# Kernel tuning notes

Measured on AMD Instinct MI355X. Metric: run time of the kernel, lower is better.

## Reference

```python
import jax, jax.numpy as jnp
import numpy as np

D_MODEL = 512
HEADS = 8
D_FF = 1024
EPS = 1e-5


def layer_norm(x, gamma, beta):
    mu = jnp.mean(x, axis=-1, keepdims=True)
    var = jnp.mean(jnp.square(x - mu), axis=-1, keepdims=True)
    return (x - mu) * jax.lax.rsqrt(var + EPS) * gamma + beta


def mha(q, k, v, mask=None):
    # q,k,v: [B, S, D]; no input/output projections in the original module
    B, Sq, D = q.shape
    Sk = k.shape[1]
    dk = D // HEADS
    qh = q.reshape(B, Sq, HEADS, dk).transpose(0, 2, 1, 3)  # [B,H,Sq,dk]
    kh = k.reshape(B, Sk, HEADS, dk).transpose(0, 2, 1, 3)
    vh = v.reshape(B, Sk, HEADS, dk).transpose(0, 2, 1, 3)
    scores = jnp.einsum('bhqd,bhkd->bhqk', qh, kh) / np.sqrt(dk).astype(q.dtype)
    if mask is not None:
        scores = jnp.where(mask == 0, jnp.asarray(-1e9, scores.dtype), scores)
    attn = jax.nn.softmax(scores, axis=-1)  # dropout is identity in eval mode
    out = jnp.einsum('bhqk,bhkd->bhqd', attn, vh)
    return out.transpose(0, 2, 1, 3).reshape(B, Sq, D)


def setup_inputs() -> dict:
    key = jax.random.key(0)
    ks = jax.random.split(key, 8)
    B, S = 4, 2048
    x = jax.random.normal(ks[0], (B, S, D_MODEL), dtype=jnp.float32)
    encoder_output = jax.random.normal(ks[1], (B, S, D_MODEL), dtype=jnp.float32)
    mask = jax.random.randint(ks[2], (B, 1, S, S), 0, 2, dtype=jnp.int32)
    params = {
        'ln1_g': jnp.ones((D_MODEL,), jnp.float32), 'ln1_b': jnp.zeros((D_MODEL,), jnp.float32),
        'ln2_g': jnp.ones((D_MODEL,), jnp.float32), 'ln2_b': jnp.zeros((D_MODEL,), jnp.float32),
        'ln3_g': jnp.ones((D_MODEL,), jnp.float32), 'ln3_b': jnp.zeros((D_MODEL,), jnp.float32),
        'W1': jax.random.normal(ks[3], (D_MODEL, D_FF), jnp.float32) * (1.0 / np.sqrt(D_MODEL)),
        'b1': jnp.zeros((D_FF,), jnp.float32),
        'W2': jax.random.normal(ks[4], (D_FF, D_MODEL), jnp.float32) * (1.0 / np.sqrt(D_FF)),
        'b2': jnp.zeros((D_MODEL,), jnp.float32),
    }
    return {'x': x, 'encoder_output': encoder_output, 'mask': mask, **params}


def reference(x, encoder_output, mask, ln1_g, ln1_b, ln2_g, ln2_b, ln3_g, ln3_b, W1, b1, W2, b2):
    # pre-norm masked self-attention + residual (dropout = identity, eval mode)
    x1 = layer_norm(x, ln1_g, ln1_b)
    x = x + mha(x1, x1, x1, mask)
    # pre-norm cross-attention + residual
    x1 = layer_norm(x, ln2_g, ln2_b)
    x = x + mha(x1, encoder_output, encoder_output, None)
    # pre-norm FFN + residual
    x1 = layer_norm(x, ln3_g, ln3_b)
    h = jax.nn.relu(x1 @ W1 + b1)
    x = x + (h @ W2 + b2)
    return x
```

## Files before the change

### kernel.cpp

```cpp
#include <hip/hip_runtime.h>
#include <hip/hip_bf16.h>

#define D_MODEL 512
#define HEADS   8
#define DK      64
#define D_FF    1024
#define SEQ     2048
#define BATCH   4
#define NTOK    (BATCH*SEQ)
#define NELEM   (NTOK*D_MODEL)

#define QSCALE  0.18033688011112042f
#define MFIX    40.0f

typedef __attribute__((ext_vector_type(8))) short bf8_t;
typedef __attribute__((ext_vector_type(4))) float f4_t;

#define GLD16(gp, lp) __builtin_amdgcn_global_load_lds( \
    (const __attribute__((address_space(1))) void*)(gp), \
    (__attribute__((address_space(3))) void*)(lp), 16, 0, 0)

__device__ __forceinline__ float ldf(const void* p, size_t i, int f32) {
    return f32 ? ((const float*)p)[i] : __bfloat162float(((const __hip_bfloat16*)p)[i]);
}
__device__ __forceinline__ short f2bf(float f) {
    union { __hip_bfloat16 h; short s; } u; u.h = __float2bfloat16(f); return u.s;
}
__device__ __forceinline__ float bf2f(short s) {
    return __uint_as_float(((unsigned)(unsigned short)s) << 16);
}
__device__ __forceinline__ unsigned fbits(float f) { return __float_as_uint(f); }

__device__ __forceinline__ float fast_exp2(float x) {
    float r; asm("v_exp_f32 %0, %1" : "=v"(r) : "v"(x)); return r;
}

__global__ void detect_k(const uint4* __restrict__ w, int* __restrict__ flags) {
    __shared__ int found;
    if (threadIdx.x == 0) found = 0;
    __syncthreads();
    int hit = 0;
    for (int i = threadIdx.x; i < 4096; i += 256) {
        uint4 u = w[i];
        if (((u.x & 0x7F80u) == 0x7F80u) || ((u.y & 0x7F80u) == 0x7F80u) ||
            ((u.z & 0x7F80u) == 0x7F80u) || ((u.w & 0x7F80u) == 0x7F80u)) hit = 1;
    }
    if (hit) atomicOr(&found, 1);
    __syncthreads();
    if (threadIdx.x == 0) flags[0] = found ? 1 : 0;
}

__device__ __forceinline__ void transpose_body(const void* src, __hip_bfloat16* dst,
                                               int K, int N, int bxi, int byi, int f32,
                                               __hip_bfloat16 (*t)[33]) {
    int bx = bxi * 32, by = byi * 32;
    int tx = threadIdx.x & 31, ty = threadIdx.x >> 5;
    #pragma unroll
    for (int j = 0; j < 32; j += 8)
        t[ty + j][tx] = __float2bfloat16(ldf(src, (size_t)(by + ty + j) * N + bx + tx, f32));
    __syncthreads();
    #pragma unroll
    for (int j = 0; j < 32; j += 8)
        dst[(size_t)(bx + ty + j) * K + by + tx] = t[tx][ty + j];
}

__global__ __launch_bounds__(256)
void prep_k(const void* __restrict__ enc, const int* __restrict__ mask,
            const void* __restrict__ W1, const void* __restrict__ W2,
            const void* __restrict__ x, const void* __restrict__ ln1g,
            const void* __restrict__ ln1b,
            const int* __restrict__ flagp,
            __hip_bfloat16* __restrict__ bufE, unsigned* __restrict__ mb,
            __hip_bfloat16* __restrict__ W1T, __hip_bfloat16* __restrict__ W2T,
            float* __restrict__ bufX, __hip_bfloat16* __restrict__ bufQ) {
    __shared__ __hip_bfloat16 t[32][33];
    int f32 = *flagp;
    int bid = blockIdx.x;
    if (bid < 16384) {
        int i = bid * 256 + threadIdx.x;
        bufE[i] = __float2bfloat16(ldf(enc, i, f32));
    } else if (bid < 18432) {
        int row  = (bid - 16384) * 4 + (threadIdx.x >> 6);
        int lane = threadIdx.x & 63;
        const int* mr = mask + (size_t)row * SEQ;
        for (int it = 0; it < SEQ/64; it++) {
            unsigned long long bal = __ballot(mr[it*64 + lane] != 0);
            if (lane == 0)  mb[(size_t)row*(SEQ/32) + it*2]     = (unsigned)bal;
            if (lane == 32) mb[(size_t)row*(SEQ/32) + it*2 + 1] = (unsigned)(bal >> 32);
        }
    } else if (bid < 18944) {
        int lb = bid - 18432;
        transpose_body(W1, W1T, D_MODEL, D_FF, lb & 31, lb >> 5, f32, t);
    } else if (bid < 19456) {
        int lb = bid - 18944;
        transpose_body(W2, W2T, D_FF, D_MODEL, lb & 15, lb >> 4, f32, t);
    } else {
        int row  = (bid - 19456) * 4 + (threadIdx.x >> 6);
        int lane = threadIdx.x & 63;
        size_t base = (size_t)row * D_MODEL;
        float v[8];
        float s = 0.f;
        #pragma unroll
        for (int i = 0; i < 8; i++) { v[i] = ldf(x, base + lane + i*64, f32); s += v[i]; }
        #pragma unroll
        for (int off = 32; off; off >>= 1) s += __shfl_xor(s, off);
        float mu = s * (1.f / D_MODEL);
        float ss = 0.f;
        #pragma unroll
        for (int i = 0; i < 8; i++) { float d = v[i] - mu; ss += d * d; }
        #pragma unroll
        for (int off = 32; off; off >>= 1) ss += __shfl_xor(ss, off);
        float rstd = rsqrtf(ss * (1.f / D_MODEL) + 1e-5f);
        #pragma unroll
        for (int i = 0; i < 8; i++) {
            int c = lane + i*64;
            bufX[base + c] = v[i];
            bufQ[base + c] = __float2bfloat16((v[i] - mu) * rstd * ldf(ln1g, c, f32) + ldf(ln1b, c, f32));
        }
    }
}

__global__ __launch_bounds__(256)
void layernorm_k(const float* __restrict__ x, const void* __restrict__ g,
                 const void* __restrict__ b, const int* __restrict__ flagp,
                 __hip_bfloat16* __restrict__ y) {
    int f32  = *flagp;
    int row  = blockIdx.x * 4 + (threadIdx.x >> 6);
    int lane = threadIdx.x & 63;
    const float* xr = x + (size_t)row * D_MODEL;
    float v[8];
    float s = 0.f;
    #pragma unroll
    for (int i = 0; i < 8; i++) { v[i] = xr[lane + i*64]; s += v[i]; }
    #pragma unroll
    for (int off = 32; off; off >>= 1) s += __shfl_xor(s, off);
    float mu = s * (1.f / D_MODEL);
    float ss = 0.f;
    #pragma unroll
    for (int i = 0; i < 8; i++) { float d = v[i] - mu; ss += d * d; }
    #pragma unroll
    for (int off = 32; off; off >>= 1) ss += __shfl_xor(ss, off);
    float rstd = rsqrtf(ss * (1.f / D_MODEL) + 1e-5f);
    __hip_bfloat16* yr = y + (size_t)row * D_MODEL;
    #pragma unroll
    for (int i = 0; i < 8; i++) {
        int c = lane + i*64;
        yr[c] = __float2bfloat16((v[i] - mu) * rstd * ldf(g, c, f32) + ldf(b, c, f32));
    }
}

__device__ __forceinline__ bf8_t prescale_q(bf8_t q) {
    bf8_t r;
    #pragma unroll
    for (int j = 0; j < 8; j++) r[j] = f2bf(bf2f(q[j]) * QSCALE);
    return r;
}

template<bool HAS_MASK>
__global__ __launch_bounds__(256, 2)
void attn_mfma_k(const __hip_bfloat16* __restrict__ Q, const __hip_bfloat16* __restrict__ K,
                 const __hip_bfloat16* __restrict__ V, const unsigned* __restrict__ mbits,
                 float* __restrict__ Xout) {
    int bid0 = blockIdx.x;
    int bid = ((bid0 & 7) << 6) | (bid0 >> 3);
    int qt = bid & 15;
    int h  = (bid >> 4) & 7;
    int b  = bid >> 7;
    int q0 = qt * 128;
    int tid  = threadIdx.x;
    int w    = tid >> 6;
    int lane = tid & 63;
    int c    = lane & 15;
    int quad = lane >> 4;

    __shared__ __hip_bfloat16 Kt[4][64 * 64];
    __shared__ __hip_bfloat16 VT[4][64 * 64];
    __shared__ __hip_bfloat16 Pb[4][2][16 * 64];

    bf8_t qf[2][2];
    #pragma unroll
    for (int g = 0; g < 2; g++) {
        const __hip_bfloat16* qrp = Q + ((size_t)(b*SEQ + q0 + 32*w + 16*g + c)) * D_MODEL + h*DK;
        qf[g][0] = prescale_q(*(const bf8_t*)(qrp + quad*8));
        qf[g][1] = prescale_q(*(const bf8_t*)(qrp + 32 + quad*8));
    }

    int kpo[4][2], vpo[4][2];
    #pragma unroll
    for (int t = 0; t < 4; t++)
        #pragma unroll
        for (int kh = 0; kh < 2; kh++) {
            int row = 16*t + c;
            kpo[t][kh] = (row*64 + (((4*kh + quad) ^ (row & 7)) * 8)) * 2;
            vpo[t][kh] = (row*64 + (((4*kh + quad) ^ (row & 7) ^ ((row >> 3) & 7)) * 8)) * 2;
        }

    int key0 = (tid >> 3) * 2, d0 = (tid & 7) * 8;
    int vtwo[8];
    #pragma unroll
    for (int j = 0; j < 8; j++) {
        int dk = d0 + j;
        int ch = (key0 >> 3) ^ (dk & 7) ^ ((dk >> 3) & 7);
        vtwo[j] = dk*128 + ch*16 + (key0 & 7)*2;
    }

    int krow[2], kc8[2];
    #pragma unroll
    for (int i = 0; i < 2; i++) {
        int idx = i*256 + tid;
        krow[i] = idx >> 3;
        kc8[i]  = ((idx & 7) ^ (krow[i] & 7)) * 8;
    }

    char* pbw[2] = { (char*)&Pb[w][0][0], (char*)&Pb[w][1][0] };
    int pwoff[4], proff[2];
    #pragma unroll
    for (int nt = 0; nt < 4; nt++)
        pwoff[nt] = c*128 + (((2*nt + (quad >> 1)) ^ (c & 7)) * 16) + (quad & 1)*8;
    #pragma unroll
    for (int kh = 0; kh < 2; kh++)
        proff[kh] = c*128 + (((4*kh + quad) ^ (c & 7)) * 16);

    const unsigned* mrp[2] = {nullptr, nullptr};
    if (HAS_MASK) {
        mrp[0] = mbits + (size_t)(b*SEQ + q0 + 32*w + c) * (SEQ/32);
        mrp[1] = mrp[0] + (size_t)16 * (SEQ/32);
    }
    int qsh = quad * 4;

    short onev = (c == 0) ? (short)0x3F80 : (short)0;
    bf8_t ones = {onev, onev, onev, onev, onev, onev, onev, onev};

    f4_t o[2][4];
    #pragma unroll
    for (int g = 0; g < 2; g++)
        #pragma unroll
        for (int mt = 0; mt < 4; mt++) o[g][mt] = (f4_t){0.f,0.f,0.f,0.f};
    f4_t l_acc[2] = {(f4_t){0.f,0.f,0.f,0.f}, (f4_t){0.f,0.f,0.f,0.f}};

    const size_t kvbase = (size_t)b * SEQ * D_MODEL + (size_t)h * DK;

    auto loadV = [&](int k0, bf8_t (&r0)[2], bf8_t (&r1)[2]) {
        #pragma unroll
        for (int t = 0; t < 2; t++) {
            const __hip_bfloat16* Vg = V + kvbase + (size_t)(k0 + t*64 + key0) * D_MODEL + d0;
            r0[t] = *(const bf8_t*)Vg;
            r1[t] = *(const bf8_t*)(Vg + D_MODEL);
        }
    };
    auto stageK = [&](int k0, int bufbase) {
        #pragma unroll
        for (int t = 0; t < 2; t++) {
            const __hip_bfloat16* Kg = K + kvbase + (size_t)(k0 + t*64) * D_MODEL;
            GLD16(Kg + (size_t)krow[0]*D_MODEL + kc8[0], (char*)&Kt[bufbase + t][0] + (w*64) * 16);
            GLD16(Kg + (size_t)krow[1]*D_MODEL + kc8[1], (char*)&Kt[bufbase + t][0] + (256 + w*64) * 16);
        }
    };
    auto writeV = [&](const bf8_t (&r0)[2], const bf8_t (&r1)[2], int bufbase) {
        #pragma unroll
        for (int t = 0; t < 2; t++) {
            const unsigned* v0u = (const unsigned*)&r0[t];
            const unsigned* v1u = (const unsigned*)&r1[t];
            char* vb = (char*)&VT[bufbase + t][0];
            #pragma unroll
            for (int dw = 0; dw < 4; dw++) {
                *(unsigned*)(vb + vtwo[2*dw])     = __builtin_amdgcn_perm(v1u[dw], v0u[dw], 0x05040100u);
                *(unsigned*)(vb + vtwo[2*dw + 1]) = __builtin_amdgcn_perm(v1u[dw], v0u[dw], 0x07060302u);
            }
        }
    };

    uint4 pm[2];
    if (HAS_MASK) { pm[0] = *(const uint4*)(mrp[0]); pm[1] = *(const uint4*)(mrp[1]); }
    bf8_t cv0[2], cv1[2];
    loadV(0, cv0, cv1);
    stageK(0, 0);
    writeV(cv0, cv1, 0);
    __syncthreads();

    for (int ph = 0; ph < SEQ/128; ph++) {
        int pb = (ph & 1) ? 2 : 0;
        int nb = pb ^ 2;

        uint4 nm[2];
        bf8_t nv0[2], nv1[2];
        if (ph < SEQ/128 - 1) {
            int kn = (ph + 1) * 128;
            if (HAS_MASK) {
                nm[0] = *(const uint4*)(mrp[0] + (kn >> 5));
                nm[1] = *(const uint4*)(mrp[1] + (kn >> 5));
            }
            loadV(kn, nv0, nv1);
            stageK(kn, nb);
        }

        #pragma unroll
        for (int t = 0; t < 2; t++) {
            const char* ktb = (const char*)&Kt[pb + t][0];
            const char* vtb = (const char*)&VT[pb + t][0];

            f4_t s[2][4];
            #pragma unroll
            for (int nt = 0; nt < 4; nt++) {
                s[0][nt] = (f4_t){-MFIX,-MFIX,-MFIX,-MFIX};
                s[1][nt] = (f4_t){-MFIX,-MFIX,-MFIX,-MFIX};
            }
            __builtin_amdgcn_s_setprio(1);
            #pragma unroll
            for (int nt = 0; nt < 4; nt++)
                #pragma unroll
                for (int kh = 0; kh < 2; kh++) {
                    bf8_t kf = *(const bf8_t*)(ktb + kpo[nt][kh]);
                    s[0][nt] = __builtin_amdgcn_mfma_f32_16x16x32_bf16(kf, qf[0][kh], s[0][nt], 0, 0, 0);
                    s[1][nt] = __builtin_amdgcn_mfma_f32_16x16x32_bf16(kf, qf[1][kh], s[1][nt], 0, 0, 0);
                }
            __builtin_amdgcn_s_setprio(0);

            #pragma unroll
            for (int g = 0; g < 2; g++) {
                unsigned wq0 = 0xffffffffu, wq1 = 0xffffffffu;
                if (HAS_MASK) {
                    wq0 = (t ? pm[g].z : pm[g].x) >> qsh;
                    wq1 = (t ? pm[g].w : pm[g].y) >> qsh;
                }
                #pragma unroll
                for (int nt = 0; nt < 4; nt++) {
                    #pragma unroll
                    for (int r = 0; r < 4; r++) {
                        float p = fast_exp2(s[g][nt][r]);
                        if (HAS_MASK) {
                            unsigned sel = (nt < 2) ? wq0 : wq1;
                            if (!((sel >> ((nt & 1)*16 + r)) & 1u)) p = 0.f;
                        }
                        s[g][nt][r] = p;
                    }
                    unsigned pk0 = __builtin_amdgcn_perm(fbits(s[g][nt][1]), fbits(s[g][nt][0]), 0x07060302u);
                    unsigned pk1 = __builtin_amdgcn_perm(fbits(s[g][nt][3]), fbits(s[g][nt][2]), 0x07060302u);
                    *(uint2*)(pbw[g] + pwoff[nt]) = make_uint2(pk0, pk1);
                }
            }

            __builtin_amdgcn_s_setprio(1);
            #pragma unroll
            for (int kh = 0; kh < 2; kh++) {
                bf8_t pfA = *(const bf8_t*)(pbw[0] + proff[kh]);
                bf8_t pfB = *(const bf8_t*)(pbw[1] + proff[kh]);
                l_acc[0] = __builtin_amdgcn_mfma_f32_16x16x32_bf16(ones, pfA, l_acc[0], 0, 0, 0);
                l_acc[1] = __builtin_amdgcn_mfma_f32_16x16x32_bf16(ones, pfB, l_acc[1], 0, 0, 0);
                #pragma unroll
                for (int mt = 0; mt < 4; mt++) {
                    bf8_t vf = *(const bf8_t*)(vtb + vpo[mt][kh]);
                    o[0][mt] = __builtin_amdgcn_mfma_f32_16x16x32_bf16(vf, pfA, o[0][mt], 0, 0, 0);
                    o[1][mt] = __builtin_amdgcn_mfma_f32_16x16x32_bf16(vf, pfB, o[1][mt], 0, 0, 0);
                }
            }
            __builtin_amdgcn_s_setprio(0);
        }

        if (ph < SEQ/128 - 1) {
            writeV(nv0, nv1, nb);
            if (HAS_MASK) { pm[0] = nm[0]; pm[1] = nm[1]; }
        }
        __syncthreads();
    }

    #pragma unroll
    for (int g = 0; g < 2; g++) {
        float lq = __shfl(l_acc[g][0], c);
        float il = 1.f / fmaxf(lq, 1e-35f);
        size_t rb = ((size_t)(b*SEQ + q0 + 32*w + 16*g + c)) * D_MODEL + h*DK;
        #pragma unroll
        for (int mt = 0; mt < 4; mt++) {
            float4* xp = (float4*)(Xout + rb + 16*mt + quad*4);
            float4 x4 = *xp;
            x4.x += o[g][mt][0] * il;
            x4.y += o[g][mt][1] * il;
            x4.z += o[g][mt][2] * il;
            x4.w += o[g][mt][3] * il;
            *xp = x4;
        }
    }
}

__global__ __launch_bounds__(256, 2)
void gemm_relu_k(const __hip_bfloat16* __restrict__ A, const __hip_bfloat16* __restrict__ BT,
                 const void* __restrict__ bias, const int* __restrict__ flagp,
                 __hip_bfloat16* __restrict__ C, int Ksz, int Nsz) {
    int f32 = *flagp;
    __shared__ __hip_bfloat16 As[2][128 * 64];
    __shared__ __hip_bfloat16 Bs[2][128 * 64];
    int tid  = threadIdx.x;
    int w    = tid >> 6;
    int c    = tid & 15;
    int quad = (tid >> 4) & 3;
    int wy = w >> 1, wx = w & 1;
    int lin = blockIdx.y * gridDim.x + blockIdx.x;
    int swz = ((lin & 7) << 6) | (lin >> 3);
    int r0 = (swz >> 3) * 128, c0 = (swz & 7) * 128;

    f4_t acc[4][4];
    #pragma unroll
    for (int i = 0; i < 4; i++)
        #pragma unroll
        for (int j = 0; j < 4; j++) acc[i][j] = (f4_t){0.f,0.f,0.f,0.f};

    auto stage = [&](int k0, int bi) {
        #pragma unroll
        for (int i = 0; i < 4; i++) {
            int idx = i*256 + tid;
            int row = idx >> 3, c8 = idx & 7;
            GLD16(A  + (size_t)(r0 + row) * Ksz + k0 + ((c8 ^ (row & 7)) * 8),
                  (char*)&As[bi][0] + (size_t)(i*256 + w*64) * 16);
            GLD16(BT + (size_t)(c0 + row) * Ksz + k0 + ((c8 ^ (row & 7)) * 8),
                  (char*)&Bs[bi][0] + (size_t)(i*256 + w*64) * 16);
        }
    };

    stage(0, 0);
    __syncthreads();
    int nk = Ksz >> 6;
    for (int ks = 0; ks < nk; ks++) {
        int bi = ks & 1;
        if (ks + 1 < nk) stage((ks + 1) << 6, bi ^ 1);

        #pragma unroll
        for (int kh = 0; kh < 2; kh++) {
            bf8_t af[4], bf[4];
            #pragma unroll
            for (int mt = 0; mt < 4; mt++) {
                int row = wy*64 + mt*16 + c;
                af[mt] = *(const bf8_t*)&As[bi][row*64 + (((kh*4 + quad) ^ (row & 7)) * 8)];
            }
            #pragma unroll
            for (int nt = 0; nt < 4; nt++) {
                int row = wx*64 + nt*16 + c;
                bf[nt] = *(const bf8_t*)&Bs[bi][row*64 + (((kh*4 + quad) ^ (row & 7)) * 8)];
            }
            #pragma unroll
            for (int mt = 0; mt < 4; mt++)
                #pragma unroll
                for (int nt = 0; nt < 4; nt++)
                    acc[mt][nt] = __builtin_amdgcn_mfma_f32_16x16x32_bf16(af[mt], bf[nt], acc[mt][nt], 0, 0, 0);
        }
        __syncthreads();
    }

    #pragma unroll
    for (int mt = 0; mt < 4; mt++)
        #pragma unroll
        for (int nt = 0; nt < 4; nt++) {
            int col = c0 + wx*64 + nt*16 + c;
            float bv = ldf(bias, col, f32);
            #pragma unroll
            for (int r = 0; r < 4; r++) {
                int m = r0 + wy*64 + mt*16 + quad*4 + r;
                C[(size_t)m * Nsz + col] = __float2bfloat16(fmaxf(acc[mt][nt][r] + bv, 0.f));
            }
        }
}

__global__ __launch_bounds__(256, 2)
void gemm_out_k(const __hip_bfloat16* __restrict__ A, const __hip_bfloat16* __restrict__ BT,
                const void* __restrict__ bias, const float* __restrict__ resid,
                const int* __restrict__ flagp, void* __restrict__ out, int Ksz, int Nsz) {
    int f32 = *flagp;
    __shared__ __hip_bfloat16 As[2][128 * 64];
    __shared__ __hip_bfloat16 Bs[2][64 * 64];
    int tid  = threadIdx.x;
    int w    = tid >> 6;
    int c    = tid & 15;
    int quad = (tid >> 4) & 3;
    int lin = blockIdx.y * gridDim.x + blockIdx.x;
    int swz = ((lin & 7) << 6) | (lin >> 3);
    int r0 = (swz >> 3) * 128, c0 = (swz & 7) * 64;

    f4_t acc[2][4];
    #pragma unroll
    for (int i = 0; i < 2; i++)
        #pragma unroll
        for (int j = 0; j < 4; j++) acc[i][j] = (f4_t){0.f,0.f,0.f,0.f};

    auto stage = [&](int k0, int bi) {
        #pragma unroll
        for (int i = 0; i < 4; i++) {
            int idx = i*256 + tid;
            int row = idx >> 3, c8 = idx & 7;
            GLD16(A + (size_t)(r0 + row) * Ksz + k0 + ((c8 ^ (row & 7)) * 8),
                  (char*)&As[bi][0] + (size_t)(i*256 + w*64) * 16);
        }
        #pragma unroll
        for (int i = 0; i < 2; i++) {
            int idx = i*256 + tid;
            int row = idx >> 3, c8 = idx & 7;
            GLD16(BT + (size_t)(c0 + row) * Ksz + k0 + ((c8 ^ (row & 7)) * 8),
                  (char*)&Bs[bi][0] + (size_t)(i*256 + w*64) * 16);
        }
    };

    stage(0, 0);
    __syncthreads();
    int nk = Ksz >> 6;
    for (int ks = 0; ks < nk; ks++) {
        int bi = ks & 1;
        if (ks + 1 < nk) stage((ks + 1) << 6, bi ^ 1);

        #pragma unroll
        for (int kh = 0; kh < 2; kh++) {
            bf8_t af[2], bf[4];
            #pragma unroll
            for (int mt = 0; mt < 2; mt++) {
                int row = w*32 + mt*16 + c;
                af[mt] = *(const bf8_t*)&As[bi][row*64 + (((kh*4 + quad) ^ (row & 7)) * 8)];
            }
            #pragma unroll
            for (int nt = 0; nt < 4; nt++) {
                int row = nt*16 + c;
                bf[nt] = *(const bf8_t*)&Bs[bi][row*64 + (((kh*4 + quad) ^ (row & 7)) * 8)];
            }
            #pragma unroll
            for (int mt = 0; mt < 2; mt++)
                #pragma unroll
                for (int nt = 0; nt < 4; nt++)
                    acc[mt][nt] = __builtin_amdgcn_mfma_f32_16x16x32_bf16(af[mt], bf[nt], acc[mt][nt], 0, 0, 0);
        }
        __syncthreads();
    }

    #pragma unroll
    for (int mt = 0; mt < 2; mt++)
        #pragma unroll
        for (int nt = 0; nt < 4; nt++) {
            int col = c0 + nt*16 + c;
            float bv = ldf(bias, col, f32);
            #pragma unroll
            for (int r = 0; r < 4; r++) {
                int m = r0 + w*32 + mt*16 + quad*4 + r;
                float v = acc[mt][nt][r] + bv + resid[(size_t)m * Nsz + col];
                if (f32) ((float*)out)[(size_t)m * Nsz + col] = v;
                else     ((__hip_bfloat16*)out)[(size_t)m * Nsz + col] = __float2bfloat16(v);
            }
        }
}

extern "C" void kernel_launch(void* const* d_in, const int* in_sizes, int n_in,
                              void* d_out, int out_size, void* d_ws, size_t ws_size,
                              hipStream_t stream) {
    const void* x    = d_in[0];
    const void* enc  = d_in[1];
    const int*  mask = (const int*)d_in[2];
    const void* ln1g = d_in[3];
    const void* ln1b = d_in[4];
    const void* ln2g = d_in[5];
    const void* ln2b = d_in[6];
    const void* ln3g = d_in[7];
    const void* ln3b = d_in[8];
    const void* W1   = d_in[9];
    const void* b1   = d_in[10];
    const void* W2   = d_in[11];
    const void* b2   = d_in[12];

    char* ws = (char*)d_ws;
    float*          bufX  = (float*)ws;
    __hip_bfloat16* bufQ  = (__hip_bfloat16*)(ws + (16u<<20));
    __hip_bfloat16* bufE  = (__hip_bfloat16*)(ws + (24u<<20));
    __hip_bfloat16* bufH  = (__hip_bfloat16*)(ws + (32u<<20));
    __hip_bfloat16* W1T   = (__hip_bfloat16*)(ws + (48u<<20));
    __hip_bfloat16* W2T   = (__hip_bfloat16*)(ws + (49u<<20));
    unsigned*       mbits = (unsigned*)(ws + (50u<<20));
    int*            flags = (int*)(ws + (52u<<20));

    dim3 blk(256);
    detect_k<<<1, blk, 0, stream>>>((const uint4*)x, flags);
    prep_k<<<21504, blk, 0, stream>>>(enc, mask, W1, W2, x, ln1g, ln1b, flags,
                                      bufE, mbits, W1T, W2T, bufX, bufQ);

    attn_mfma_k<true><<<BATCH*HEADS*(SEQ/128), blk, 0, stream>>>(bufQ, bufQ, bufQ, mbits, bufX);
    layernorm_k<<<NTOK/4, blk, 0, stream>>>(bufX, ln2g, ln2b, flags, bufQ);
    attn_mfma_k<false><<<BATCH*HEADS*(SEQ/128), blk, 0, stream>>>(bufQ, bufE, bufE, nullptr, bufX);
    layernorm_k<<<NTOK/4, blk, 0, stream>>>(bufX, ln3g, ln3b, flags, bufQ);
    gemm_relu_k<<<dim3(D_FF/128, NTOK/128), blk, 0, stream>>>(bufQ, W1T, b1, flags, bufH, D_MODEL, D_FF);
    gemm_out_k<<<dim3(D_MODEL/64, NTOK/128), blk, 0, stream>>>(bufH, W2T, b2, bufX, flags, d_out, D_FF, D_MODEL);
}
```

Before: 330.3 us.

## Shrink attention tiles to 64 queries per block and raise occupancy

The attention kernel now gives each block 64 query rows (16 per wave instead of 32) and streams K/V in 64-key phases with double buffering instead of 128. LDS per block and registers per thread drop, and launch bounds go from 2 to 4 blocks per CU, doubling the grid to 1024 blocks. This trades fewer MFMAs per K/V fragment load, and twice as many K/V global reads and barriers, for more waves in flight to hide latency.

```diff
diff --git a/kernel.cpp b/kernel.cpp
--- a/kernel.cpp
+++ b/kernel.cpp
@@ -157,32 +157,31 @@
 }
 
 template<bool HAS_MASK>
-__global__ __launch_bounds__(256, 2)
+__global__ __launch_bounds__(256, 4)
 void attn_mfma_k(const __hip_bfloat16* __restrict__ Q, const __hip_bfloat16* __restrict__ K,
                  const __hip_bfloat16* __restrict__ V, const unsigned* __restrict__ mbits,
                  float* __restrict__ Xout) {
     int bid0 = blockIdx.x;
-    int bid = ((bid0 & 7) << 6) | (bid0 >> 3);
-    int qt = bid & 15;
-    int h  = (bid >> 4) & 7;
-    int b  = bid >> 7;
-    int q0 = qt * 128;
+    int bid = ((bid0 & 7) << 7) | (bid0 >> 3);
+    int qt = bid & 31;
+    int h  = (bid >> 5) & 7;
+    int b  = bid >> 8;
+    int q0 = qt * 64;
     int tid  = threadIdx.x;
     int w    = tid >> 6;
     int lane = tid & 63;
     int c    = lane & 15;
     int quad = lane >> 4;
 
-    __shared__ __hip_bfloat16 Kt[4][64 * 64];
-    __shared__ __hip_bfloat16 VT[4][64 * 64];
-    __shared__ __hip_bfloat16 Pb[4][2][16 * 64];
-
-    bf8_t qf[2][2];
-    #pragma unroll
-    for (int g = 0; g < 2; g++) {
-        const __hip_bfloat16* qrp = Q + ((size_t)(b*SEQ + q0 + 32*w + 16*g + c)) * D_MODEL + h*DK;
-        qf[g][0] = prescale_q(*(const bf8_t*)(qrp + quad*8));
-        qf[g][1] = prescale_q(*(const bf8_t*)(qrp + 32 + quad*8));
+    __shared__ __hip_bfloat16 Kt[2][64 * 64];
+    __shared__ __hip_bfloat16 VT[2][64 * 64];
+    __shared__ __hip_bfloat16 Pb[4][16 * 64];
+
+    bf8_t qf[2];
+    {
+        const __hip_bfloat16* qrp = Q + ((size_t)(b*SEQ + q0 + 16*w + c)) * D_MODEL + h*DK;
+        qf[0] = prescale_q(*(const bf8_t*)(qrp + quad*8));
+        qf[1] = prescale_q(*(const bf8_t*)(qrp + 32 + quad*8));
     }
 
     int kpo[4][2], vpo[4][2];
@@ -212,7 +211,7 @@
         kc8[i]  = ((idx & 7) ^ (krow[i] & 7)) * 8;
     }
 
-    char* pbw[2] = { (char*)&Pb[w][0][0], (char*)&Pb[w][1][0] };
+    char* pbw = (char*)&Pb[w][0];
     int pwoff[4], proff[2];
     #pragma unroll
     for (int nt = 0; nt < 4; nt++)
@@ -221,162 +220,132 @@
     for (int kh = 0; kh < 2; kh++)
         proff[kh] = c*128 + (((4*kh + quad) ^ (c & 7)) * 16);
 
-    const unsigned* mrp[2] = {nullptr, nullptr};
-    if (HAS_MASK) {
-        mrp[0] = mbits + (size_t)(b*SEQ + q0 + 32*w + c) * (SEQ/32);
-        mrp[1] = mrp[0] + (size_t)16 * (SEQ/32);
-    }
+    const unsigned* mrp = nullptr;
+    if (HAS_MASK)
+        mrp = mbits + (size_t)(b*SEQ + q0 + 16*w + c) * (SEQ/32);
     int qsh = quad * 4;
 
     short onev = (c == 0) ? (short)0x3F80 : (short)0;
     bf8_t ones = {onev, onev, onev, onev, onev, onev, onev, onev};
 
-    f4_t o[2][4];
-    #pragma unroll
-    for (int g = 0; g < 2; g++)
-        #pragma unroll
-        for (int mt = 0; mt < 4; mt++) o[g][mt] = (f4_t){0.f,0.f,0.f,0.f};
-    f4_t l_acc[2] = {(f4_t){0.f,0.f,0.f,0.f}, (f4_t){0.f,0.f,0.f,0.f}};
+    f4_t o[4];
+    #pragma unroll
+    for (int mt = 0; mt < 4; mt++) o[mt] = (f4_t){0.f,0.f,0.f,0.f};
+    f4_t l_acc = (f4_t){0.f,0.f,0.f,0.f};
 
     const size_t kvbase = (size_t)b * SEQ * D_MODEL + (size_t)h * DK;
 
-    auto loadV = [&](int k0, bf8_t (&r0)[2], bf8_t (&r1)[2]) {
-        #pragma unroll
-        for (int t = 0; t < 2; t++) {
-            const __hip_bfloat16* Vg = V + kvbase + (size_t)(k0 + t*64 + key0) * D_MODEL + d0;
-            r0[t] = *(const bf8_t*)Vg;
-            r1[t] = *(const bf8_t*)(Vg + D_MODEL);
-        }
+    auto loadV = [&](int k0, bf8_t& r0, bf8_t& r1) {
+        const __hip_bfloat16* Vg = V + kvbase + (size_t)(k0 + key0) * D_MODEL + d0;
+        r0 = *(const bf8_t*)Vg;
+        r1 = *(const bf8_t*)(Vg + D_MODEL);
     };
-    auto stageK = [&](int k0, int bufbase) {
-        #pragma unroll
-        for (int t = 0; t < 2; t++) {
-            const __hip_bfloat16* Kg = K + kvbase + (size_t)(k0 + t*64) * D_MODEL;
-            GLD16(Kg + (size_t)krow[0]*D_MODEL + kc8[0], (char*)&Kt[bufbase + t][0] + (w*64) * 16);
-            GLD16(Kg + (size_t)krow[1]*D_MODEL + kc8[1], (char*)&Kt[bufbase + t][0] + (256 + w*64) * 16);
-        }
+    auto stageK = [&](int k0, int bi) {
+        const __hip_bfloat16* Kg = K + kvbase + (size_t)k0 * D_MODEL;
+        GLD16(Kg + (size_t)krow[0]*D_MODEL + kc8[0], (char*)&Kt[bi][0] + (w*64) * 16);
+        GLD16(Kg + (size_t)krow[1]*D_MODEL + kc8[1], (char*)&Kt[bi][0] + (256 + w*64) * 16);
     };
-    auto writeV = [&](const bf8_t (&r0)[2], const bf8_t (&r1)[2], int bufbase) {
-        #pragma unroll
-        for (int t = 0; t < 2; t++) {
-            const unsigned* v0u = (const unsigned*)&r0[t];
-            const unsigned* v1u = (const unsigned*)&r1[t];
-            char* vb = (char*)&VT[bufbase + t][0];
-            #pragma unroll
-            for (int dw = 0; dw < 4; dw++) {
-                *(unsigned*)(vb + vtwo[2*dw])     = __builtin_amdgcn_perm(v1u[dw], v0u[dw], 0x05040100u);
-                *(unsigned*)(vb + vtwo[2*dw + 1]) = __builtin_amdgcn_perm(v1u[dw], v0u[dw], 0x07060302u);
-            }
+    auto writeV = [&](const bf8_t& r0, const bf8_t& r1, int bi) {
+        const unsigned* v0u = (const unsigned*)&r0;
+        const unsigned* v1u = (const unsigned*)&r1;
+        char* vb = (char*)&VT[bi][0];
+        #pragma unroll
+        for (int dw = 0; dw < 4; dw++) {
+            *(unsigned*)(vb + vtwo[2*dw])     = __builtin_amdgcn_perm(v1u[dw], v0u[dw], 0x05040100u);
+            *(unsigned*)(vb + vtwo[2*dw + 1]) = __builtin_amdgcn_perm(v1u[dw], v0u[dw], 0x07060302u);
         }
     };
 
-    uint4 pm[2];
-    if (HAS_MASK) { pm[0] = *(const uint4*)(mrp[0]); pm[1] = *(const uint4*)(mrp[1]); }
-    bf8_t cv0[2], cv1[2];
+    uint2 pm;
+    if (HAS_MASK) pm = *(const uint2*)(mrp);
+    bf8_t cv0, cv1;
     loadV(0, cv0, cv1);
     stageK(0, 0);
     writeV(cv0, cv1, 0);
     __syncthreads();
 
-    for (int ph = 0; ph < SEQ/128; ph++) {
-        int pb = (ph & 1) ? 2 : 0;
-        int nb = pb ^ 2;
-
-        uint4 nm[2];
-        bf8_t nv0[2], nv1[2];
-        if (ph < SEQ/128 - 1) {
-            int kn = (ph + 1) * 128;
-            if (HAS_MASK) {
-                nm[0] = *(const uint4*)(mrp[0] + (kn >> 5));
-                nm[1] = *(const uint4*)(mrp[1] + (kn >> 5));
-            }
+    for (int ph = 0; ph < SEQ/64; ph++) {
+        int bi = ph & 1;
+        int ni = bi ^ 1;
+
+        uint2 nm;
+        bf8_t nv0, nv1;
+        if (ph < SEQ/64 - 1) {
+            int kn = (ph + 1) * 64;
+            if (HAS_MASK) nm = *(const uint2*)(mrp + (kn >> 5));
             loadV(kn, nv0, nv1);
-            stageK(kn, nb);
-        }
-
-        #pragma unroll
-        for (int t = 0; t < 2; t++) {
-            const char* ktb = (const char*)&Kt[pb + t][0];
-            const char* vtb = (const char*)&VT[pb + t][0];
-
-            f4_t s[2][4];
-            #pragma unroll
-            for (int nt = 0; nt < 4; nt++) {
-                s[0][nt] = (f4_t){-MFIX,-MFIX,-MFIX,-MFIX};
-                s[1][nt] = (f4_t){-MFIX,-MFIX,-MFIX,-MFIX};
-            }
+            stageK(kn, ni);
+        }
+
+        {
+            const char* ktb = (const char*)&Kt[bi][0];
+            const char* vtb = (const char*)&VT[bi][0];
+
+            f4_t s[4];
+            #pragma unroll
+            for (int nt = 0; nt < 4; nt++)
+                s[nt] = (f4_t){-MFIX,-MFIX,-MFIX,-MFIX};
             __builtin_amdgcn_s_setprio(1);
             #pragma unroll
             for (int nt = 0; nt < 4; nt++)
                 #pragma unroll
                 for (int kh = 0; kh < 2; kh++) {
                     bf8_t kf = *(const bf8_t*)(ktb + kpo[nt][kh]);
-                    s[0][nt] = __builtin_amdgcn_mfma_f32_16x16x32_bf16(kf, qf[0][kh], s[0][nt], 0, 0, 0);
-                    s[1][nt] = __builtin_amdgcn_mfma_f32_16x16x32_bf16(kf, qf[1][kh], s[1][nt], 0, 0, 0);
+                    s[nt] = __builtin_amdgcn_mfma_f32_16x16x32_bf16(kf, qf[kh], s[nt], 0, 0, 0);
                 }
             __builtin_amdgcn_s_setprio(0);
 
-            #pragma unroll
-            for (int g = 0; g < 2; g++) {
-                unsigned wq0 = 0xffffffffu, wq1 = 0xffffffffu;
-                if (HAS_MASK) {
-                    wq0 = (t ? pm[g].z : pm[g].x) >> qsh;
-                    wq1 = (t ? pm[g].w : pm[g].y) >> qsh;
+            unsigned wq0 = 0xffffffffu, wq1 = 0xffffffffu;
+            if (HAS_MASK) { wq0 = pm.x >> qsh; wq1 = pm.y >> qsh; }
+            #pragma unroll
+            for (int nt = 0; nt < 4; nt++) {
+                #pragma unroll
+                for (int r = 0; r < 4; r++) {
+                    float p = fast_exp2(s[nt][r]);
+                    if (HAS_MASK) {
+                        unsigned sel = (nt < 2) ? wq0 : wq1;
+                        if (!((sel >> ((nt & 1)*16 + r)) & 1u)) p = 0.f;
+                    }
+                    s[nt][r] = p;
                 }
-                #pragma unroll
-                for (int nt = 0; nt < 4; nt++) {
-                    #pragma unroll
-                    for (int r = 0; r < 4; r++) {
-                        float p = fast_exp2(s[g][nt][r]);
-                        if (HAS_MASK) {
-                            unsigned sel = (nt < 2) ? wq0 : wq1;
-                            if (!((sel >> ((nt & 1)*16 + r)) & 1u)) p = 0.f;
-                        }
-                        s[g][nt][r] = p;
-                    }
-                    unsigned pk0 = __builtin_amdgcn_perm(fbits(s[g][nt][1]), fbits(s[g][nt][0]), 0x07060302u);
-                    unsigned pk1 = __builtin_amdgcn_perm(fbits(s[g][nt][3]), fbits(s[g][nt][2]), 0x07060302u);
-                    *(uint2*)(pbw[g] + pwoff[nt]) = make_uint2(pk0, pk1);
-                }
+                unsigned pk0 = __builtin_amdgcn_perm(fbits(s[nt][1]), fbits(s[nt][0]), 0x07060302u);
+                unsigned pk1 = __builtin_amdgcn_perm(fbits(s[nt][3]), fbits(s[nt][2]), 0x07060302u);
+                *(uint2*)(pbw + pwoff[nt]) = make_uint2(pk0, pk1);
             }
 
             __builtin_amdgcn_s_setprio(1);
             #pragma unroll
             for (int kh = 0; kh < 2; kh++) {
-                bf8_t pfA = *(const bf8_t*)(pbw[0] + proff[kh]);
-                bf8_t pfB = *(const bf8_t*)(pbw[1] + proff[kh]);
-                l_acc[0] = __builtin_amdgcn_mfma_f32_16x16x32_bf16(ones, pfA, l_acc[0], 0, 0, 0);
-                l_acc[1] = __builtin_amdgcn_mfma_f32_16x16x32_bf16(ones, pfB, l_acc[1], 0, 0, 0);
+                bf8_t pf = *(const bf8_t*)(pbw + proff[kh]);
+                l_acc = __builtin_amdgcn_mfma_f32_16x16x32_bf16(ones, pf, l_acc, 0, 0, 0);
                 #pragma unroll
                 for (int mt = 0; mt < 4; mt++) {
                     bf8_t vf = *(const bf8_t*)(vtb + vpo[mt][kh]);
-                    o[0][mt] = __builtin_amdgcn_mfma_f32_16x16x32_bf16(vf, pfA, o[0][mt], 0, 0, 0);
-                    o[1][mt] = __builtin_amdgcn_mfma_f32_16x16x32_bf16(vf, pfB, o[1][mt], 0, 0, 0);
+                    o[mt] = __builtin_amdgcn_mfma_f32_16x16x32_bf16(vf, pf, o[mt], 0, 0, 0);
                 }
             }
             __builtin_amdgcn_s_setprio(0);
         }
 
-        if (ph < SEQ/128 - 1) {
-            writeV(nv0, nv1, nb);
-            if (HAS_MASK) { pm[0] = nm[0]; pm[1] = nm[1]; }
+        if (ph < SEQ/64 - 1) {
+            writeV(nv0, nv1, ni);
+            if (HAS_MASK) pm = nm;
         }
         __syncthreads();
     }
 
-    #pragma unroll
-    for (int g = 0; g < 2; g++) {
-        float lq = __shfl(l_acc[g][0], c);
+    {
+        float lq = __shfl(l_acc[0], c);
         float il = 1.f / fmaxf(lq, 1e-35f);
-        size_t rb = ((size_t)(b*SEQ + q0 + 32*w + 16*g + c)) * D_MODEL + h*DK;
+        size_t rb = ((size_t)(b*SEQ + q0 + 16*w + c)) * D_MODEL + h*DK;
         #pragma unroll
         for (int mt = 0; mt < 4; mt++) {
             float4* xp = (float4*)(Xout + rb + 16*mt + quad*4);
             float4 x4 = *xp;
-            x4.x += o[g][mt][0] * il;
-            x4.y += o[g][mt][1] * il;
-            x4.z += o[g][mt][2] * il;
-            x4.w += o[g][mt][3] * il;
+            x4.x += o[mt][0] * il;
+            x4.y += o[mt][1] * il;
+            x4.z += o[mt][2] * il;
+            x4.w += o[mt][3] * il;
             *xp = x4;
         }
     }
@@ -574,9 +543,9 @@
     prep_k<<<21504, blk, 0, stream>>>(enc, mask, W1, W2, x, ln1g, ln1b, flags,
                                       bufE, mbits, W1T, W2T, bufX, bufQ);
 
-    attn_mfma_k<true><<<BATCH*HEADS*(SEQ/128), blk, 0, stream>>>(bufQ, bufQ, bufQ, mbits, bufX);
+    attn_mfma_k<true><<<BATCH*HEADS*(SEQ/64), blk, 0, stream>>>(bufQ, bufQ, bufQ, mbits, bufX);
     layernorm_k<<<NTOK/4, blk, 0, stream>>>(bufX, ln2g, ln2b, flags, bufQ);
-    attn_mfma_k<false><<<BATCH*HEADS*(SEQ/128), blk, 0, stream>>>(bufQ, bufE, bufE, nullptr, bufX);
+    attn_mfma_k<false><<<BATCH*HEADS*(SEQ/64), blk, 0, stream>>>(bufQ, bufE, bufE, nullptr, bufX);
     layernorm_k<<<NTOK/4, blk, 0, stream>>>(bufX, ln3g, ln3b, flags, bufQ);
     gemm_relu_k<<<dim3(D_FF/128, NTOK/128), blk, 0, stream>>>(bufQ, W1T, b1, flags, bufH, D_MODEL, D_FF);
     gemm_out_k<<<dim3(D_MODEL/64, NTOK/128), blk, 0, stream>>>(bufH, W2T, b2, bufX, flags, d_out, D_FF, D_MODEL);
```

Result: slower. 344.5 us (+4.3%).

## Fold dtype detection into prep kernel and vectorize prep and layernorm memory access

Applied to the files above, without the earlier changes.

Removes the separate single-block detect kernel: each prep block now probes the input dtype itself. The encoder-conversion and LN1 paths switch to 8-element vector loads and stores, which shrinks the prep grid. Small parameters (LN gains and biases, FFN biases) are pre-converted to bf16 once so later kernels skip the per-element flag branch. The risks are redundant probe reads in every block, and bf16 rounding of gamma, beta and the biases, which slightly changes numerics.

```diff
diff --git a/kernel.cpp b/kernel.cpp
--- a/kernel.cpp
+++ b/kernel.cpp
@@ -35,19 +35,19 @@
     float r; asm("v_exp_f32 %0, %1" : "=v"(r) : "v"(x)); return r;
 }
 
-__global__ void detect_k(const uint4* __restrict__ w, int* __restrict__ flags) {
-    __shared__ int found;
-    if (threadIdx.x == 0) found = 0;
-    __syncthreads();
+__device__ __forceinline__ int probe_f32(const uint4* __restrict__ xq, int* sh) {
+    if (threadIdx.x == 0) *sh = 0;
     int hit = 0;
-    for (int i = threadIdx.x; i < 4096; i += 256) {
-        uint4 u = w[i];
+    #pragma unroll
+    for (int i = 0; i < 8; i++) {
+        uint4 u = xq[i*256 + threadIdx.x];
         if (((u.x & 0x7F80u) == 0x7F80u) || ((u.y & 0x7F80u) == 0x7F80u) ||
             ((u.z & 0x7F80u) == 0x7F80u) || ((u.w & 0x7F80u) == 0x7F80u)) hit = 1;
     }
-    if (hit) atomicOr(&found, 1);
     __syncthreads();
-    if (threadIdx.x == 0) flags[0] = found ? 1 : 0;
+    if (hit) atomicOr(sh, 1);
+    __syncthreads();
+    return *sh;
 }
 
 __device__ __forceinline__ void transpose_body(const void* src, __hip_bfloat16* dst,
@@ -67,20 +67,33 @@
 __global__ __launch_bounds__(256)
 void prep_k(const void* __restrict__ enc, const int* __restrict__ mask,
             const void* __restrict__ W1, const void* __restrict__ W2,
-            const void* __restrict__ x, const void* __restrict__ ln1g,
-            const void* __restrict__ ln1b,
-            const int* __restrict__ flagp,
+            const void* __restrict__ x,
+            const void* __restrict__ ln1g, const void* __restrict__ ln1b,
+            const void* __restrict__ ln2g, const void* __restrict__ ln2b,
+            const void* __restrict__ ln3g, const void* __restrict__ ln3b,
+            const void* __restrict__ b1,   const void* __restrict__ b2,
             __hip_bfloat16* __restrict__ bufE, unsigned* __restrict__ mb,
             __hip_bfloat16* __restrict__ W1T, __hip_bfloat16* __restrict__ W2T,
-            float* __restrict__ bufX, __hip_bfloat16* __restrict__ bufQ) {
+            float* __restrict__ bufX, __hip_bfloat16* __restrict__ bufQ,
+            __hip_bfloat16* __restrict__ pbuf, int* __restrict__ flags) {
     __shared__ __hip_bfloat16 t[32][33];
-    int f32 = *flagp;
+    __shared__ int shf;
+    int f32 = probe_f32((const uint4*)x, &shf);
     int bid = blockIdx.x;
-    if (bid < 16384) {
-        int i = bid * 256 + threadIdx.x;
-        bufE[i] = __float2bfloat16(ldf(enc, i, f32));
-    } else if (bid < 18432) {
-        int row  = (bid - 16384) * 4 + (threadIdx.x >> 6);
+    if (bid < 2048) {
+        size_t i0 = ((size_t)bid * 256 + threadIdx.x) * 8;
+        bf8_t o8;
+        if (f32) {
+            const float4* ep = (const float4*)((const float*)enc + i0);
+            float4 a = ep[0], b4 = ep[1];
+            o8[0]=f2bf(a.x);  o8[1]=f2bf(a.y);  o8[2]=f2bf(a.z);  o8[3]=f2bf(a.w);
+            o8[4]=f2bf(b4.x); o8[5]=f2bf(b4.y); o8[6]=f2bf(b4.z); o8[7]=f2bf(b4.w);
+        } else {
+            o8 = *(const bf8_t*)((const __hip_bfloat16*)enc + i0);
+        }
+        *(bf8_t*)(bufE + i0) = o8;
+    } else if (bid < 4096) {
+        int row  = (bid - 2048) * 4 + (threadIdx.x >> 6);
         int lane = threadIdx.x & 63;
         const int* mr = mask + (size_t)row * SEQ;
         for (int it = 0; it < SEQ/64; it++) {
@@ -88,20 +101,31 @@
             if (lane == 0)  mb[(size_t)row*(SEQ/32) + it*2]     = (unsigned)bal;
             if (lane == 32) mb[(size_t)row*(SEQ/32) + it*2 + 1] = (unsigned)(bal >> 32);
         }
-    } else if (bid < 18944) {
-        int lb = bid - 18432;
+    } else if (bid < 4608) {
+        int lb = bid - 4096;
         transpose_body(W1, W1T, D_MODEL, D_FF, lb & 31, lb >> 5, f32, t);
-    } else if (bid < 19456) {
-        int lb = bid - 18944;
+    } else if (bid < 5120) {
+        int lb = bid - 4608;
         transpose_body(W2, W2T, D_FF, D_MODEL, lb & 15, lb >> 4, f32, t);
-    } else {
-        int row  = (bid - 19456) * 4 + (threadIdx.x >> 6);
+    } else if (bid < 7168) {
+        int row  = (bid - 5120) * 4 + (threadIdx.x >> 6);
         int lane = threadIdx.x & 63;
+        int c0   = lane * 8;
         size_t base = (size_t)row * D_MODEL;
         float v[8];
+        if (f32) {
+            const float4* xp = (const float4*)((const float*)x + base + c0);
+            float4 a = xp[0], b4 = xp[1];
+            v[0]=a.x; v[1]=a.y; v[2]=a.z; v[3]=a.w;
+            v[4]=b4.x; v[5]=b4.y; v[6]=b4.z; v[7]=b4.w;
+        } else {
+            bf8_t x8 = *(const bf8_t*)((const __hip_bfloat16*)x + base + c0);
+            #pragma unroll
+            for (int j = 0; j < 8; j++) v[j] = bf2f(x8[j]);
+        }
         float s = 0.f;
         #pragma unroll
-        for (int i = 0; i < 8; i++) { v[i] = ldf(x, base + lane + i*64, f32); s += v[i]; }
+        for (int i = 0; i < 8; i++) s += v[i];
         #pragma unroll
         for (int off = 32; off; off >>= 1) s += __shfl_xor(s, off);
         float mu = s * (1.f / D_MODEL);
@@ -111,27 +135,43 @@
         #pragma unroll
         for (int off = 32; off; off >>= 1) ss += __shfl_xor(ss, off);
         float rstd = rsqrtf(ss * (1.f / D_MODEL) + 1e-5f);
-        #pragma unroll
-        for (int i = 0; i < 8; i++) {
-            int c = lane + i*64;
-            bufX[base + c] = v[i];
-            bufQ[base + c] = __float2bfloat16((v[i] - mu) * rstd * ldf(ln1g, c, f32) + ldf(ln1b, c, f32));
-        }
+        *(float4*)(bufX + base + c0)     = make_float4(v[0], v[1], v[2], v[3]);
+        *(float4*)(bufX + base + c0 + 4) = make_float4(v[4], v[5], v[6], v[7]);
+        bf8_t q8;
+        #pragma unroll
+        for (int j = 0; j < 8; j++)
+            q8[j] = f2bf((v[j] - mu) * rstd * ldf(ln1g, c0 + j, f32) + ldf(ln1b, c0 + j, f32));
+        *(bf8_t*)(bufQ + base + c0) = q8;
+    } else {
+        int i = threadIdx.x;
+        if (i < 128 || i >= 0) {
+            for (int k = i; k < 512; k += 256) {
+                pbuf[k]        = __float2bfloat16(ldf(ln2g, k, f32));
+                pbuf[512 + k]  = __float2bfloat16(ldf(ln2b, k, f32));
+                pbuf[1024 + k] = __float2bfloat16(ldf(ln3g, k, f32));
+                pbuf[1536 + k] = __float2bfloat16(ldf(ln3b, k, f32));
+                pbuf[3072 + k] = __float2bfloat16(ldf(b2, k, f32));
+            }
+            for (int k = i; k < 1024; k += 256)
+                pbuf[2048 + k] = __float2bfloat16(ldf(b1, k, f32));
+        }
+        if (i == 0) flags[0] = f32;
     }
 }
 
 __global__ __launch_bounds__(256)
-void layernorm_k(const float* __restrict__ x, const void* __restrict__ g,
-                 const void* __restrict__ b, const int* __restrict__ flagp,
+void layernorm_k(const float* __restrict__ x, const __hip_bfloat16* __restrict__ g,
+                 const __hip_bfloat16* __restrict__ b,
                  __hip_bfloat16* __restrict__ y) {
-    int f32  = *flagp;
     int row  = blockIdx.x * 4 + (threadIdx.x >> 6);
     int lane = threadIdx.x & 63;
-    const float* xr = x + (size_t)row * D_MODEL;
-    float v[8];
+    int c0   = lane * 8;
+    const float4* xp = (const float4*)(x + (size_t)row * D_MODEL + c0);
+    float4 a = xp[0], b4 = xp[1];
+    float v[8] = {a.x, a.y, a.z, a.w, b4.x, b4.y, b4.z, b4.w};
     float s = 0.f;
     #pragma unroll
-    for (int i = 0; i < 8; i++) { v[i] = xr[lane + i*64]; s += v[i]; }
+    for (int i = 0; i < 8; i++) s += v[i];
     #pragma unroll
     for (int off = 32; off; off >>= 1) s += __shfl_xor(s, off);
     float mu = s * (1.f / D_MODEL);
@@ -141,12 +181,13 @@
     #pragma unroll
     for (int off = 32; off; off >>= 1) ss += __shfl_xor(ss, off);
     float rstd = rsqrtf(ss * (1.f / D_MODEL) + 1e-5f);
-    __hip_bfloat16* yr = y + (size_t)row * D_MODEL;
-    #pragma unroll
-    for (int i = 0; i < 8; i++) {
-        int c = lane + i*64;
-        yr[c] = __float2bfloat16((v[i] - mu) * rstd * ldf(g, c, f32) + ldf(b, c, f32));
-    }
+    bf8_t g8 = *(const bf8_t*)(g + c0);
+    bf8_t b8 = *(const bf8_t*)(b + c0);
+    bf8_t y8;
+    #pragma unroll
+    for (int j = 0; j < 8; j++)
+        y8[j] = f2bf((v[j] - mu) * rstd * bf2f(g8[j]) + bf2f(b8[j]));
+    *(bf8_t*)(y + (size_t)row * D_MODEL + c0) = y8;
 }
 
 __device__ __forceinline__ bf8_t prescale_q(bf8_t q) {
@@ -384,9 +425,8 @@
 
 __global__ __launch_bounds__(256, 2)
 void gemm_relu_k(const __hip_bfloat16* __restrict__ A, const __hip_bfloat16* __restrict__ BT,
-                 const void* __restrict__ bias, const int* __restrict__ flagp,
+                 const __hip_bfloat16* __restrict__ bias,
                  __hip_bfloat16* __restrict__ C, int Ksz, int Nsz) {
-    int f32 = *flagp;
     __shared__ __hip_bfloat16 As[2][128 * 64];
     __shared__ __hip_bfloat16 Bs[2][128 * 64];
     int tid  = threadIdx.x;
@@ -450,7 +490,7 @@
         #pragma unroll
         for (int nt = 0; nt < 4; nt++) {
             int col = c0 + wx*64 + nt*16 + c;
-            float bv = ldf(bias, col, f32);
+            float bv = __bfloat162float(bias[col]);
             #pragma unroll
             for (int r = 0; r < 4; r++) {
                 int m = r0 + wy*64 + mt*16 + quad*4 + r;
@@ -461,7 +501,7 @@
 
 __global__ __launch_bounds__(256, 2)
 void gemm_out_k(const __hip_bfloat16* __restrict__ A, const __hip_bfloat16* __restrict__ BT,
-                const void* __restrict__ bias, const float* __restrict__ resid,
+                const __hip_bfloat16* __restrict__ bias, const float* __restrict__ resid,
                 const int* __restrict__ flagp, void* __restrict__ out, int Ksz, int Nsz) {
     int f32 = *flagp;
     __shared__ __hip_bfloat16 As[2][128 * 64];
@@ -531,7 +571,7 @@
         #pragma unroll
         for (int nt = 0; nt < 4; nt++) {
             int col = c0 + nt*16 + c;
-            float bv = ldf(bias, col, f32);
+            float bv = __bfloat162float(bias[col]);
             #pragma unroll
             for (int r = 0; r < 4; r++) {
                 int m = r0 + w*32 + mt*16 + quad*4 + r;
@@ -568,16 +608,17 @@
     __hip_bfloat16* W2T   = (__hip_bfloat16*)(ws + (49u<<20));
     unsigned*       mbits = (unsigned*)(ws + (50u<<20));
     int*            flags = (int*)(ws + (52u<<20));
+    __hip_bfloat16* pbuf  = (__hip_bfloat16*)(ws + (52u<<20) + 4096);
 
     dim3 blk(256);
-    detect_k<<<1, blk, 0, stream>>>((const uint4*)x, flags);
-    prep_k<<<21504, blk, 0, stream>>>(enc, mask, W1, W2, x, ln1g, ln1b, flags,
-                                      bufE, mbits, W1T, W2T, bufX, bufQ);
+    prep_k<<<7169, blk, 0, stream>>>(enc, mask, W1, W2, x, ln1g, ln1b,
+                                     ln2g, ln2b, ln3g, ln3b, b1, b2,
+                                     bufE, mbits, W1T, W2T, bufX, bufQ, pbuf, flags);
 
     attn_mfma_k<true><<<BATCH*HEADS*(SEQ/128), blk, 0, stream>>>(bufQ, bufQ, bufQ, mbits, bufX);
-    layernorm_k<<<NTOK/4, blk, 0, stream>>>(bufX, ln2g, ln2b, flags, bufQ);
+    layernorm_k<<<NTOK/4, blk, 0, stream>>>(bufX, pbuf, pbuf + 512, bufQ);
     attn_mfma_k<false><<<BATCH*HEADS*(SEQ/128), blk, 0, stream>>>(bufQ, bufE, bufE, nullptr, bufX);
-    layernorm_k<<<NTOK/4, blk, 0, stream>>>(bufX, ln3g, ln3b, flags, bufQ);
-    gemm_relu_k<<<dim3(D_FF/128, NTOK/128), blk, 0, stream>>>(bufQ, W1T, b1, flags, bufH, D_MODEL, D_FF);
-    gemm_out_k<<<dim3(D_MODEL/64, NTOK/128), blk, 0, stream>>>(bufH, W2T, b2, bufX, flags, d_out, D_FF, D_MODEL);
-}
+    layernorm_k<<<NTOK/4, blk, 0, stream>>>(bufX, pbuf + 1024, pbuf + 1536, bufQ);
+    gemm_relu_k<<<dim3(D_FF/128, NTOK/128), blk, 0, stream>>>(bufQ, W1T, pbuf + 2048, bufH, D_MODEL, D_FF);
+    gemm_out_k<<<dim3(D_MODEL/64, NTOK/128), blk, 0, stream>>>(bufH, W2T, pbuf + 3072, bufX, flags, d_out, D_FF, D_MODEL);
+}
```

Result: slower. 347.9 us (+5.3%).
